# Optimization experiments

Hardware: AMD Instinct MI355X
Metric: run time of the kernel (lower is better)

## Reference

```python
import jax, jax.numpy as jnp
import numpy as np

POOL = 2  # pooling_size == pooling_stride == 2, SAME padding, H even -> no actual pad


def setup_inputs() -> dict:
    key = jax.random.key(0)
    k1, k2 = jax.random.split(key)
    B, H, C = 8, 28, 32
    mu_in = jax.random.normal(k1, (B, H, H, C), dtype=jnp.float32)
    # per-channel spatial covariance: [B, H*H, H*H, C]
    Sigma_in = jax.random.uniform(k2, (B, H * H, H * H, C), dtype=jnp.float32)
    return {"mu_in": mu_in, "Sigma_in": Sigma_in}


def reference(mu_in, Sigma_in):
    B, H, W, C = mu_in.shape
    ho, wo = H // POOL, W // POOL
    # non-overlapping 2x2 windows, row-major within window (matches TF argmax order)
    patches = mu_in.reshape(B, ho, POOL, wo, POOL, C).transpose(0, 1, 3, 2, 4, 5)
    patches = patches.reshape(B, ho, wo, POOL * POOL, C)
    mu_out = jnp.max(patches, axis=3)                     # [B, ho, wo, C]
    k = jnp.argmax(patches, axis=3)                       # [B, ho, wo, C], first-match ties like TF
    dy, dx = k // POOL, k % POOL
    iy = POOL * jnp.arange(ho)[None, :, None, None] + dy  # input row of the max
    ix = POOL * jnp.arange(wo)[None, None, :, None] + dx  # input col of the max
    # TF decode: index = y*hw_in + x  (flat spatial index in the input image)
    index = (iy * W + ix).astype(jnp.int32)               # [B, ho, wo, C]
    index = index.transpose(0, 3, 1, 2).reshape(B, C, ho * wo)  # [B, C, N_out]
    # Sigma: [B, N_in, N_in, C] -> [B, C, N_in, N_in], then double gather
    S1 = Sigma_in.transpose(0, 3, 1, 2)
    g1 = jnp.take_along_axis(S1, index[:, :, :, None], axis=2)       # [B, C, N_out, N_in]
    Sigma_out = jnp.take_along_axis(g1, index[:, :, None, :], axis=3)  # [B, C, N_out, N_out]
    Sigma_out = Sigma_out.transpose(0, 2, 3, 1)           # [B, N_out, N_out, C]
    return mu_out, Sigma_out
```

## Files before the change

kernel.cpp:

```cpp
#include <hip/hip_runtime.h>
#include <stdint.h>

#define BATCH 8
#define HIN   28
#define CH    32
#define HO    14
#define NIN   784
#define NOUT  196
#define ROW_W   (NIN * CH)
#define JH      392
#define STAGE_W (JH * CH)
#define NCHUNK  49
#define TILE_W  (NOUT * CH)

typedef float f32x4 __attribute__((ext_vector_type(4)));

#if defined(__has_builtin)
#if __has_builtin(__builtin_amdgcn_global_load_lds)
#define HAS_GLDS 1
#endif
#endif

__global__ __launch_bounds__(1024, 8) void vdp_pool_dma_kernel(
        const float* __restrict__ mu_in,
        const float* __restrict__ sigma_in,
        float* __restrict__ mu_out,
        float* __restrict__ sigma_out)
{
    __shared__ __align__(16) float stage[STAGE_W];
    __shared__ uint16_t colsel[TILE_W];

    const int bid = blockIdx.x;
    const int jh  = bid & 1;
    const int bp  = bid >> 1;
    const int b   = bp / NOUT;
    const int p   = bp - b * NOUT;
    const int tid = threadIdx.x;

    if (tid < NOUT * 2) {
        const int q2 = tid >> 1, hf = tid & 1;
        const int qy = q2 / HO, qx = q2 - qy * HO;
        const float* base =
            mu_in + (((size_t)b * HIN + 2 * qy) * HIN + 2 * qx) * CH + hf * 16;
        const int jb = (2 * qy) * HIN + 2 * qx;

        #pragma unroll
        for (int g = 0; g < 4; ++g) {
            const float4 v0 = *(const float4*)(base + g * 4);
            const float4 v1 = *(const float4*)(base + CH + g * 4);
            const float4 v2 = *(const float4*)(base + HIN * CH + g * 4);
            const float4 v3 = *(const float4*)(base + HIN * CH + CH + g * 4);
            float m0, m1, m2, m3;
            uint32_t k0, k1, k2, k3;
            { float best = v0.x; uint32_t k = 0;
              if (v1.x > best) { best = v1.x; k = 1; }
              if (v2.x > best) { best = v2.x; k = 2; }
              if (v3.x > best) { best = v3.x; k = 3; }
              m0 = best; k0 = k; }
            { float best = v0.y; uint32_t k = 0;
              if (v1.y > best) { best = v1.y; k = 1; }
              if (v2.y > best) { best = v2.y; k = 2; }
              if (v3.y > best) { best = v3.y; k = 3; }
              m1 = best; k1 = k; }
            { float best = v0.z; uint32_t k = 0;
              if (v1.z > best) { best = v1.z; k = 1; }
              if (v2.z > best) { best = v2.z; k = 2; }
              if (v3.z > best) { best = v3.z; k = 3; }
              m2 = best; k2 = k; }
            { float best = v0.w; uint32_t k = 0;
              if (v1.w > best) { best = v1.w; k = 1; }
              if (v2.w > best) { best = v2.w; k = 2; }
              if (v3.w > best) { best = v3.w; k = 3; }
              m3 = best; k3 = k; }
            const int cb = q2 * CH + hf * 16 + g * 4;
            colsel[cb + 0] = (uint16_t)(jb + (int)(k0 >> 1) * HIN + (int)(k0 & 1));
            colsel[cb + 1] = (uint16_t)(jb + (int)(k1 >> 1) * HIN + (int)(k1 & 1));
            colsel[cb + 2] = (uint16_t)(jb + (int)(k2 >> 1) * HIN + (int)(k2 & 1));
            colsel[cb + 3] = (uint16_t)(jb + (int)(k3 >> 1) * HIN + (int)(k3 & 1));
            if (q2 == p) {
                *(float4*)(mu_out + (size_t)bp * CH + hf * 16 + g * 4) =
                    make_float4(m0, m1, m2, m3);
            }
        }
    }
    __syncthreads();

    const int c    = tid & 31;
    const int qb0  = tid >> 5;
    const int lane = tid & 63;
    const int wave = tid >> 6;
    const int jlo  = jh * JH;

    uint16_t jcol[7];
    #pragma unroll
    for (int k = 0; k < 7; ++k) {
        const int q = qb0 + 32 * k;
        jcol[k] = (q < NOUT) ? colsel[q * CH + c] : (uint16_t)0;
    }
    const int jrow = (int)colsel[p * CH + c];

    const int py = p / HO, px = p - py * HO;
    float acc[7] = {0, 0, 0, 0, 0, 0, 0};

    for (int r = 0; r < 4; ++r) {
        const int i_r = (2 * py + (r >> 1)) * HIN + 2 * px + (r & 1);
        const float* rowb =
            sigma_in + ((size_t)b * NIN + i_r) * ROW_W + (size_t)jlo * CH;

#ifdef HAS_GLDS
        #pragma unroll
        for (int k = 0; k < 4; ++k) {
            const int ck = wave + 16 * k;
            if (ck < NCHUNK)
                __builtin_amdgcn_global_load_lds(
                    (const __attribute__((address_space(1))) void*)
                        (rowb + ck * 256 + lane * 4),
                    (__attribute__((address_space(3))) void*)
                        (stage + ck * 256 + lane * 4),
                    16, 0, 0);
        }
#else
        f32x4 tmp[4];
        #pragma unroll
        for (int k = 0; k < 4; ++k) {
            const int ck = wave + 16 * k;
            tmp[k] = (ck < NCHUNK)
                ? *(const f32x4*)(rowb + ck * 256 + lane * 4)
                : (f32x4){0, 0, 0, 0};
        }
        #pragma unroll
        for (int k = 0; k < 4; ++k) {
            const int ck = wave + 16 * k;
            if (ck < NCHUNK)
                *(f32x4*)(stage + ck * 256 + lane * 4) = tmp[k];
        }
#endif
        __syncthreads();

        const bool rhit = (jrow == i_r);
        #pragma unroll
        for (int k = 0; k < 7; ++k) {
            const int jl    = (int)jcol[k] - jlo;
            const bool mine = (jl >= 0) && (jl < JH);
            const int  ja   = mine ? jl : 0;
            const float v   = stage[ja * CH + c];
            acc[k] = (rhit && mine) ? v : acc[k];
        }
        __syncthreads();
    }

    float* ob = sigma_out + (size_t)bp * TILE_W;
    #pragma unroll
    for (int k = 0; k < 7; ++k) {
        const int q  = qb0 + 32 * k;
        const int jl = (int)jcol[k] - jlo;
        if (q < NOUT && jl >= 0 && jl < JH)
            __builtin_nontemporal_store(acc[k], ob + q * CH + c);
    }
}

extern "C" void kernel_launch(void* const* d_in, const int* in_sizes, int n_in,
                              void* d_out, int out_size, void* d_ws, size_t ws_size,
                              hipStream_t stream) {
    const float* mu_in    = (const float*)d_in[0];
    const float* sigma_in = (const float*)d_in[1];

    float* mu_out    = (float*)d_out;
    float* sigma_out = (float*)d_out + BATCH * NOUT * CH;

    vdp_pool_dma_kernel<<<BATCH * NOUT * 2, 1024, 0, stream>>>(
        mu_in, sigma_in, mu_out, sigma_out);
}
```

Baseline: 132.1 us.

## Double-buffer sigma row staging with async LDS loads overlapping gather

Splits each block's half-row of Sigma into two 196-column stages and double-buffers them in LDS. It issues the next stage's global-to-LDS DMA before processing the current one, and uses vmcnt waits and raw s_barrier instead of full syncs. The first load is issued before the mu pooling/argmax phase so that phase hides load latency. LDS per block stays similar, but the launch-bounds occupancy hint drops from 8 to 2 and there are now 8 barrier-separated stages instead of 4.

```diff
diff --git a/kernel.cpp b/kernel.cpp
--- a/kernel.cpp
+++ b/kernel.cpp
@@ -7,27 +7,21 @@
 #define HO    14
 #define NIN   784
 #define NOUT  196
-#define ROW_W   (NIN * CH)
-#define JH      392
-#define STAGE_W (JH * CH)
-#define NCHUNK  49
-#define TILE_W  (NOUT * CH)
+#define ROW_W (NIN * CH)
+#define JH    392
+#define JS    196
+#define STG_W (JS * CH)
+#define TILE_W (NOUT * CH)
 
 typedef float f32x4 __attribute__((ext_vector_type(4)));
 
-#if defined(__has_builtin)
-#if __has_builtin(__builtin_amdgcn_global_load_lds)
-#define HAS_GLDS 1
-#endif
-#endif
-
-__global__ __launch_bounds__(1024, 8) void vdp_pool_dma_kernel(
+__global__ __launch_bounds__(1024, 2) void vdp_pool_pipe_kernel(
         const float* __restrict__ mu_in,
         const float* __restrict__ sigma_in,
         float* __restrict__ mu_out,
         float* __restrict__ sigma_out)
 {
-    __shared__ __align__(16) float stage[STAGE_W];
+    __shared__ __align__(16) float buf[2][STG_W];
     __shared__ uint16_t colsel[TILE_W];
 
     const int bid = blockIdx.x;
@@ -36,6 +30,41 @@
     const int b   = bp / NOUT;
     const int p   = bp - b * NOUT;
     const int tid = threadIdx.x;
+    const int w   = tid >> 6;
+    const int l   = tid & 63;
+    const int py  = p / HO, px = p - py * HO;
+
+    auto issue = [&](int s) {
+        const int rr  = s >> 1;
+        const int i_r = (2 * py + (rr >> 1)) * HIN + 2 * px + (rr & 1);
+        const float* src = sigma_in + ((size_t)b * NIN + i_r) * ROW_W
+                         + (size_t)(jh * JH + (s & 1) * JS) * CH;
+        float* dst = buf[s & 1];
+        if (w < 10) {
+            __builtin_amdgcn_global_load_lds(
+                (const __attribute__((address_space(1))) void*)(src + w * 512 + l * 4),
+                (__attribute__((address_space(3))) void*)(dst + w * 512 + l * 4),
+                16, 0, 0);
+            __builtin_amdgcn_global_load_lds(
+                (const __attribute__((address_space(1))) void*)(src + w * 512 + 256 + l * 4),
+                (__attribute__((address_space(3))) void*)(dst + w * 512 + 256 + l * 4),
+                16, 0, 0);
+        } else if (w < 14) {
+            const int off = 5120 + (w - 10) * 256;
+            __builtin_amdgcn_global_load_lds(
+                (const __attribute__((address_space(1))) void*)(src + off + l * 4),
+                (__attribute__((address_space(3))) void*)(dst + off + l * 4),
+                16, 0, 0);
+        } else {
+            const int off = 6144 + (w - 14) * 64;
+            __builtin_amdgcn_global_load_lds(
+                (const __attribute__((address_space(1))) void*)(src + off + l),
+                (__attribute__((address_space(3))) void*)(dst + off + l),
+                4, 0, 0);
+        }
+    };
+
+    issue(0);
 
     if (tid < NOUT * 2) {
         const int q2 = tid >> 1, hf = tid & 1;
@@ -85,11 +114,8 @@
     }
     __syncthreads();
 
-    const int c    = tid & 31;
-    const int qb0  = tid >> 5;
-    const int lane = tid & 63;
-    const int wave = tid >> 6;
-    const int jlo  = jh * JH;
+    const int c   = tid & 31;
+    const int qb0 = tid >> 5;
 
     uint16_t jcol[7];
     #pragma unroll
@@ -99,62 +125,46 @@
     }
     const int jrow = (int)colsel[p * CH + c];
 
-    const int py = p / HO, px = p - py * HO;
     float acc[7] = {0, 0, 0, 0, 0, 0, 0};
 
-    for (int r = 0; r < 4; ++r) {
-        const int i_r = (2 * py + (r >> 1)) * HIN + 2 * px + (r & 1);
-        const float* rowb =
-            sigma_in + ((size_t)b * NIN + i_r) * ROW_W + (size_t)jlo * CH;
+    #pragma unroll
+    for (int s = 0; s < 8; ++s) {
+        if (s < 7) issue(s + 1);
+        if (s == 7) {
+            asm volatile("s_waitcnt vmcnt(0)" ::: "memory");
+        } else if (w < 10) {
+            asm volatile("s_waitcnt vmcnt(2)" ::: "memory");
+        } else {
+            asm volatile("s_waitcnt vmcnt(1)" ::: "memory");
+        }
+        __builtin_amdgcn_sched_barrier(0);
+        asm volatile("s_barrier" ::: "memory");
+        __builtin_amdgcn_sched_barrier(0);
 
-#ifdef HAS_GLDS
-        #pragma unroll
-        for (int k = 0; k < 4; ++k) {
-            const int ck = wave + 16 * k;
-            if (ck < NCHUNK)
-                __builtin_amdgcn_global_load_lds(
-                    (const __attribute__((address_space(1))) void*)
-                        (rowb + ck * 256 + lane * 4),
-                    (__attribute__((address_space(3))) void*)
-                        (stage + ck * 256 + lane * 4),
-                    16, 0, 0);
-        }
-#else
-        f32x4 tmp[4];
-        #pragma unroll
-        for (int k = 0; k < 4; ++k) {
-            const int ck = wave + 16 * k;
-            tmp[k] = (ck < NCHUNK)
-                ? *(const f32x4*)(rowb + ck * 256 + lane * 4)
-                : (f32x4){0, 0, 0, 0};
-        }
-        #pragma unroll
-        for (int k = 0; k < 4; ++k) {
-            const int ck = wave + 16 * k;
-            if (ck < NCHUNK)
-                *(f32x4*)(stage + ck * 256 + lane * 4) = tmp[k];
-        }
-#endif
-        __syncthreads();
-
+        const int rr  = s >> 1;
+        const int i_r = (2 * py + (rr >> 1)) * HIN + 2 * px + (rr & 1);
+        const int jsl = jh * JH + (s & 1) * JS;
+        const float* bpB = buf[s & 1];
         const bool rhit = (jrow == i_r);
         #pragma unroll
         for (int k = 0; k < 7; ++k) {
-            const int jl    = (int)jcol[k] - jlo;
-            const bool mine = (jl >= 0) && (jl < JH);
-            const int  ja   = mine ? jl : 0;
-            const float v   = stage[ja * CH + c];
+            const int  jl   = (int)jcol[k] - jsl;
+            const bool mine = (unsigned)jl < (unsigned)JS;
+            const float v   = bpB[(mine ? jl : 0) * CH + c];
             acc[k] = (rhit && mine) ? v : acc[k];
         }
-        __syncthreads();
+        asm volatile("s_waitcnt lgkmcnt(0)" ::: "memory");
+        __builtin_amdgcn_sched_barrier(0);
+        asm volatile("s_barrier" ::: "memory");
+        __builtin_amdgcn_sched_barrier(0);
     }
 
     float* ob = sigma_out + (size_t)bp * TILE_W;
     #pragma unroll
     for (int k = 0; k < 7; ++k) {
         const int q  = qb0 + 32 * k;
-        const int jl = (int)jcol[k] - jlo;
-        if (q < NOUT && jl >= 0 && jl < JH)
+        const int jl = (int)jcol[k] - jh * JH;
+        if (q < NOUT && (unsigned)jl < (unsigned)JH)
             __builtin_nontemporal_store(acc[k], ob + q * CH + c);
     }
 }
@@ -168,6 +178,6 @@
     float* mu_out    = (float*)d_out;
     float* sigma_out = (float*)d_out + BATCH * NOUT * CH;
 
-    vdp_pool_dma_kernel<<<BATCH * NOUT * 2, 1024, 0, stream>>>(
+    vdp_pool_pipe_kernel<<<BATCH * NOUT * 2, 1024, 0, stream>>>(
         mu_in, sigma_in, mu_out, sigma_out);
 }
```

Result: slower. 145.7 us (+10.3%).
